# Optimization experiments

Measured on AMD Instinct MI355X. Metric: run time of the kernel, lower is better.

Reference implementation:

```python
import jax, jax.numpy as jnp
import numpy as np

D = 256; HEADS = 8; LVLS = 4; PTS = 4; NLAYERS = 6; DFF = 1024
SHAPES = [(64, 64), (32, 32), (16, 16), (8, 8)]
B = 4
N = sum(h * w for h, w in SHAPES)  # 5440


def setup_inputs() -> dict:
    key = jax.random.key(0)
    ks = jax.random.split(key, 24)
    L = NLAYERS
    w = lambda k, *s: jax.random.normal(k, s, jnp.float32) * 0.02
    inp = {}
    inp['src'] = jax.random.normal(ks[0], (B, N, D), jnp.float32)
    inp['pos'] = jax.random.normal(ks[1], (B, N, D), jnp.float32) * 0.02
    inp['valid_ratios'] = jnp.ones((B, LVLS, 2), jnp.float32)
    inp['spatial_shapes'] = jnp.array(SHAPES, jnp.int32)
    lsi = np.cumsum([0] + [h * w_ for h, w_ in SHAPES])[:-1]
    inp['level_start_index'] = jnp.array(lsi, jnp.int32)
    inp['W_off'] = w(ks[2], L, D, HEADS * LVLS * PTS * 2)
    inp['b_off'] = jax.random.normal(ks[3], (L, HEADS * LVLS * PTS * 2), jnp.float32) * 0.5
    inp['W_attn'] = w(ks[4], L, D, HEADS * LVLS * PTS)
    inp['b_attn'] = jnp.zeros((L, HEADS * LVLS * PTS), jnp.float32)
    inp['W_val'] = w(ks[5], L, D, D)
    inp['b_val'] = jnp.zeros((L, D), jnp.float32)
    inp['W_out'] = w(ks[6], L, D, D)
    inp['b_out'] = jnp.zeros((L, D), jnp.float32)
    inp['g1'] = jnp.ones((L, D), jnp.float32)
    inp['be1'] = jnp.zeros((L, D), jnp.float32)
    inp['W1'] = w(ks[7], L, D, DFF)
    inp['bl1'] = jnp.zeros((L, DFF), jnp.float32)
    inp['W2'] = w(ks[8], L, DFF, D)
    inp['bl2'] = jnp.zeros((L, D), jnp.float32)
    inp['g2'] = jnp.ones((L, D), jnp.float32)
    inp['be2'] = jnp.zeros((L, D), jnp.float32)
    return inp


def layernorm(x, g, b):
    m = x.mean(-1, keepdims=True)
    v = ((x - m) ** 2).mean(-1, keepdims=True)
    return (x - m) * jax.lax.rsqrt(v + 1e-5) * g + b


def get_ref(valid_ratios):
    refs = []
    for lvl, (H_, W_) in enumerate(SHAPES):
        ry, rx = jnp.meshgrid(jnp.linspace(0.5, H_ - 0.5, H_), jnp.linspace(0.5, W_ - 0.5, W_), indexing='ij')
        ry = ry.reshape(-1)[None] / (valid_ratios[:, None, lvl, 1] * H_)
        rx = rx.reshape(-1)[None] / (valid_ratios[:, None, lvl, 0] * W_)
        refs.append(jnp.stack([rx, ry], -1))
    ref = jnp.concatenate(refs, 1)           # [B, N, 2]
    return ref[:, :, None] * valid_ratios[:, None]  # [B, N, L, 2]


def msda(query, value_in, ref, Woff, boff, Wat, bat, Wv, bv, Wo, bo):
    # Standard Deformable-DETR MSDeformAttn (bilinear gather + weighted sum).
    Bq, Q, _ = query.shape
    Dh = D // HEADS
    value = (value_in @ Wv + bv).reshape(Bq, -1, HEADS, Dh).transpose(0, 2, 1, 3)  # [B,H,N,Dh]
    off = (query @ Woff + boff).reshape(Bq, Q, HEADS, LVLS, PTS, 2)
    attn = jax.nn.softmax((query @ Wat + bat).reshape(Bq, Q, HEADS, LVLS * PTS), -1)
    attn = attn.reshape(Bq, Q, HEADS, LVLS, PTS)
    norm = jnp.array([[w_, h_] for h_, w_ in SHAPES], query.dtype)  # (W_, H_) per level
    loc = ref[:, :, None, :, None, :] + off / norm[None, None, None, :, None, :]
    out = jnp.zeros((Bq, Q, HEADS, Dh), query.dtype)
    start = 0
    for lvl, (H_, W_) in enumerate(SHAPES):
        v = value[:, :, start:start + H_ * W_]  # [B,H,HW,Dh]
        start += H_ * W_
        l = loc[:, :, :, lvl]                    # [B,Q,H,P,2] in [0,1]
        x = l[..., 0] * W_ - 0.5
        y = l[..., 1] * H_ - 0.5
        x0 = jnp.floor(x); y0 = jnp.floor(y)
        fx = x - x0; fy = y - y0
        x0i = x0.astype(jnp.int32); y0i = y0.astype(jnp.int32)

        def g(xi, yi):
            valid = ((xi >= 0) & (xi < W_) & (yi >= 0) & (yi < H_)).astype(query.dtype)
            idx = jnp.clip(yi, 0, H_ - 1) * W_ + jnp.clip(xi, 0, W_ - 1)
            it = idx.transpose(0, 2, 1, 3).reshape(Bq, HEADS, -1)  # [B,H,Q*P]
            got = jnp.take_along_axis(v, it[..., None], axis=2)    # [B,H,Q*P,Dh]
            got = got.reshape(Bq, HEADS, Q, PTS, Dh).transpose(0, 2, 1, 3, 4)
            return got * valid[..., None]

        samp = (g(x0i, y0i) * ((1 - fx) * (1 - fy))[..., None]
                + g(x0i + 1, y0i) * (fx * (1 - fy))[..., None]
                + g(x0i, y0i + 1) * ((1 - fx) * fy)[..., None]
                + g(x0i + 1, y0i + 1) * (fx * fy)[..., None])  # [B,Q,H,P,Dh]
        out = out + jnp.einsum('bqhp,bqhpd->bqhd', attn[:, :, :, lvl], samp)
    return out.reshape(Bq, Q, D) @ Wo + bo


def reference(src, pos, valid_ratios, spatial_shapes, level_start_index,
              W_off, b_off, W_attn, b_attn, W_val, b_val, W_out, b_out,
              g1, be1, W1, bl1, W2, bl2, g2, be2):
    ref = get_ref(valid_ratios)
    out = src
    for i in range(NLAYERS):
        q = out + pos
        x2 = msda(q, out, ref, W_off[i], b_off[i], W_attn[i], b_attn[i],
                  W_val[i], b_val[i], W_out[i], b_out[i])
        out = layernorm(out + x2, g1[i], be1[i])
        ffn = jax.nn.relu(out @ W1[i] + bl1[i]) @ W2[i] + bl2[i]
        out = layernorm(out + ffn, g2[i], be2[i])
    return out
```

## Files before the change

### kernel.cpp

```cpp
#include <hip/hip_runtime.h>
#include <math.h>

#define B_   4
#define N_   5440
#define D_   256
#define M_   21760
#define NL_  6
#define MH_  10880

typedef unsigned short us16;
typedef unsigned int   u32;
typedef __attribute__((ext_vector_type(8))) short  short8v;
typedef __attribute__((ext_vector_type(4))) float  f32x4;

__device__ __forceinline__ float b2f(us16 u) {
  return __uint_as_float(((u32)u) << 16);
}
__device__ __forceinline__ int iclip(int v, int lo, int hi) {
  return v < lo ? lo : (v > hi ? hi : v);
}

__global__ __launch_bounds__(256) void split_wT(const float* __restrict__ W,
                                                us16* __restrict__ out,
                                                int K, int N, int ld, int rowOff) {
  const int idx = blockIdx.x * 256 + threadIdx.x;
  const int k = idx % K;
  const int n = (idx / K) % N;
  const int l = idx / (K * N);
  const float x = W[(size_t)l * K * N + (size_t)k * N + n];
  const u32 u = __float_as_uint(x);
  const us16 hi = (us16)(u >> 16);
  const float rem = x - __uint_as_float(u & 0xFFFF0000u);
  const us16 lo = (us16)(__float_as_uint(rem) >> 16);
  us16* o = out + (size_t)l * ld * 2 * K + (size_t)(rowOff + n) * 2 * K;
  o[k] = hi;
  o[K + k] = lo;
}


__global__ __launch_bounds__(256) void gemm_qkv(
    const float* __restrict__ X, const float* __restrict__ P,
    const us16* __restrict__ BT,
    const float* __restrict__ bVal, const float* __restrict__ bOff,
    const float* __restrict__ bAttn,
    float* __restrict__ val, us16* __restrict__ off16,
    us16* __restrict__ attnl16) {
  __shared__ __align__(16) us16 Ah[128 * 72];
  __shared__ __align__(16) us16 Al[128 * 72];
  __shared__ __align__(16) us16 Bh[128 * 72];
  __shared__ __align__(16) us16 Bl[128 * 72];
  const int tid  = threadIdx.x;
  const int row0 = blockIdx.y * 128;
  const int col0 = blockIdx.x * 128;
  const bool useAdd = (col0 >= 256);
  const int l  = tid & 63;
  const int w  = tid >> 6;
  const int wr = (w >> 1) * 64;
  const int wc = (w & 1) * 64;
  const int lg = l >> 4;
  const int lr = l & 15;
  const int K = 256;

  f32x4 acc[4][4];
#pragma unroll
  for (int m = 0; m < 4; ++m)
#pragma unroll
    for (int n = 0; n < 4; ++n)
#pragma unroll
      for (int j = 0; j < 4; ++j) acc[m][n][j] = 0.f;

  for (int t = 0; t < 4; ++t) {
    const int kB = t << 6;
    __syncthreads();
#pragma unroll
    for (int r = 0; r < 4; ++r) {
      const int id = r * 256 + tid;
      const int row = id >> 3;
      const int cg = id & 7;
      const float* src = &X[(size_t)(row0 + row) * K + kB + cg * 8];
      float4 f0 = *(const float4*)src;
      float4 f1 = *(const float4*)(src + 4);
      if (useAdd) {
        const float* s2 = &P[(size_t)(row0 + row) * K + kB + cg * 8];
        float4 g0 = *(const float4*)s2;
        float4 g1 = *(const float4*)(s2 + 4);
        f0.x += g0.x; f0.y += g0.y; f0.z += g0.z; f0.w += g0.w;
        f1.x += g1.x; f1.y += g1.y; f1.z += g1.z; f1.w += g1.w;
      }
      const float xs[8] = {f0.x, f0.y, f0.z, f0.w, f1.x, f1.y, f1.z, f1.w};
      union { us16 u[8]; uint4 v; } ph, pl;
#pragma unroll
      for (int j = 0; j < 8; ++j) {
        const u32 u = __float_as_uint(xs[j]);
        ph.u[j] = (us16)(u >> 16);
        const float rem = xs[j] - __uint_as_float(u & 0xFFFF0000u);
        pl.u[j] = (us16)(__float_as_uint(rem) >> 16);
      }
      *(uint4*)&Ah[row * 72 + cg * 8] = ph.v;
      *(uint4*)&Al[row * 72 + cg * 8] = pl.v;
    }
#pragma unroll
    for (int r = 0; r < 4; ++r) {
      const int id = r * 256 + tid;
      const int row = id >> 3;
      const int cg = id & 7;
      const us16* brow = &BT[(size_t)(col0 + row) * 512];
      *(uint4*)&Bh[row * 72 + cg * 8] = *(const uint4*)&brow[kB + cg * 8];
      *(uint4*)&Bl[row * 72 + cg * 8] = *(const uint4*)&brow[K + kB + cg * 8];
    }
    __syncthreads();
#pragma unroll
    for (int kk = 0; kk < 2; ++kk) {
      const int ko = kk * 32 + lg * 8;
      short8v ah[4], bb[4], cc[4];
#pragma unroll
      for (int mf = 0; mf < 4; ++mf)
        ah[mf] = *(const short8v*)&Ah[(wr + mf * 16 + lr) * 72 + ko];
#pragma unroll
      for (int nf = 0; nf < 4; ++nf)
        bb[nf] = *(const short8v*)&Bh[(wc + nf * 16 + lr) * 72 + ko];
#pragma unroll
      for (int mf = 0; mf < 4; ++mf)
#pragma unroll
        for (int nf = 0; nf < 4; ++nf)
          acc[mf][nf] = __builtin_amdgcn_mfma_f32_16x16x32_bf16(ah[mf], bb[nf], acc[mf][nf], 0, 0, 0);
#pragma unroll
      for (int nf = 0; nf < 4; ++nf)
        cc[nf] = *(const short8v*)&Bl[(wc + nf * 16 + lr) * 72 + ko];
#pragma unroll
      for (int mf = 0; mf < 4; ++mf)
#pragma unroll
        for (int nf = 0; nf < 4; ++nf)
          acc[mf][nf] = __builtin_amdgcn_mfma_f32_16x16x32_bf16(ah[mf], cc[nf], acc[mf][nf], 0, 0, 0);
#pragma unroll
      for (int mf = 0; mf < 4; ++mf)
        ah[mf] = *(const short8v*)&Al[(wr + mf * 16 + lr) * 72 + ko];
#pragma unroll
      for (int mf = 0; mf < 4; ++mf)
#pragma unroll
        for (int nf = 0; nf < 4; ++nf)
          acc[mf][nf] = __builtin_amdgcn_mfma_f32_16x16x32_bf16(ah[mf], bb[nf], acc[mf][nf], 0, 0, 0);
    }
  }
  float* Cf = nullptr; us16* Ch = nullptr;
  const float* bp; int ldc, csub;
  if (col0 < 256)      { Cf = val;     bp = bVal;  ldc = 256; csub = 0;   }
  else if (col0 < 512) { Ch = off16;   bp = bOff;  ldc = 256; csub = 256; }
  else                 { Ch = attnl16; bp = bAttn; ldc = 128; csub = 512; }
#pragma unroll
  for (int mf = 0; mf < 4; ++mf) {
#pragma unroll
    for (int nf = 0; nf < 4; ++nf) {
      const int cc2 = col0 + wc + nf * 16 + lr - csub;
      const float bvv = bp[cc2];
#pragma unroll
      for (int j = 0; j < 4; ++j) {
        const int row = row0 + wr + mf * 16 + lg * 4 + j;
        const float v = acc[mf][nf][j] + bvv;
        if (Ch) Ch[(size_t)row * ldc + cc2] = (us16)(__float_as_uint(v) >> 16);
        else    Cf[(size_t)row * ldc + cc2] = v;
      }
    }
  }
}

__global__ __launch_bounds__(256) void gemm_split(
    const float* __restrict__ A,
    const us16* __restrict__ BT, const float* __restrict__ bias,
    float* __restrict__ C0, float* __restrict__ C1,
    int Kfull, int kLen, int N, int relu) {
  __shared__ __align__(16) us16 Ah[128 * 72];
  __shared__ __align__(16) us16 Al[128 * 72];
  __shared__ __align__(16) us16 Bh[128 * 72];
  __shared__ __align__(16) us16 Bl[128 * 72];
  const int tid  = threadIdx.x;
  const int row0 = blockIdx.y * 128;
  const int col0 = blockIdx.x * 128;
  const int kOff = blockIdx.z * kLen;
  const int l  = tid & 63;
  const int w  = tid >> 6;
  const int wr = (w >> 1) * 64;
  const int wc = (w & 1) * 64;
  const int lg = l >> 4;
  const int lr = l & 15;

  f32x4 acc[4][4];
#pragma unroll
  for (int m = 0; m < 4; ++m)
#pragma unroll
    for (int n = 0; n < 4; ++n)
#pragma unroll
      for (int j = 0; j < 4; ++j) acc[m][n][j] = 0.f;

  const int T = kLen >> 6;
  for (int t = 0; t < T; ++t) {
    const int kB = kOff + (t << 6);
    __syncthreads();
#pragma unroll
    for (int r = 0; r < 4; ++r) {
      const int id = r * 256 + tid;
      const int row = id >> 3;
      const int cg = id & 7;
      const float* src = &A[(size_t)(row0 + row) * Kfull + kB + cg * 8];
      const float4 f0 = *(const float4*)src;
      const float4 f1 = *(const float4*)(src + 4);
      const float xs[8] = {f0.x, f0.y, f0.z, f0.w, f1.x, f1.y, f1.z, f1.w};
      union { us16 u[8]; uint4 v; } ph, pl;
#pragma unroll
      for (int j = 0; j < 8; ++j) {
        const u32 u = __float_as_uint(xs[j]);
        ph.u[j] = (us16)(u >> 16);
        const float rem = xs[j] - __uint_as_float(u & 0xFFFF0000u);
        pl.u[j] = (us16)(__float_as_uint(rem) >> 16);
      }
      *(uint4*)&Ah[row * 72 + cg * 8] = ph.v;
      *(uint4*)&Al[row * 72 + cg * 8] = pl.v;
    }
#pragma unroll
    for (int r = 0; r < 4; ++r) {
      const int id = r * 256 + tid;
      const int row = id >> 3;
      const int cg = id & 7;
      const us16* brow = &BT[(size_t)(col0 + row) * 2 * Kfull];
      *(uint4*)&Bh[row * 72 + cg * 8] = *(const uint4*)&brow[kB + cg * 8];
      *(uint4*)&Bl[row * 72 + cg * 8] = *(const uint4*)&brow[Kfull + kB + cg * 8];
    }
    __syncthreads();
#pragma unroll
    for (int kk = 0; kk < 2; ++kk) {
      const int ko = kk * 32 + lg * 8;
      short8v ah[4], bb[4], cc[4];
#pragma unroll
      for (int mf = 0; mf < 4; ++mf)
        ah[mf] = *(const short8v*)&Ah[(wr + mf * 16 + lr) * 72 + ko];
#pragma unroll
      for (int nf = 0; nf < 4; ++nf)
        bb[nf] = *(const short8v*)&Bh[(wc + nf * 16 + lr) * 72 + ko];
#pragma unroll
      for (int mf = 0; mf < 4; ++mf)
#pragma unroll
        for (int nf = 0; nf < 4; ++nf)
          acc[mf][nf] = __builtin_amdgcn_mfma_f32_16x16x32_bf16(ah[mf], bb[nf], acc[mf][nf], 0, 0, 0);
#pragma unroll
      for (int nf = 0; nf < 4; ++nf)
        cc[nf] = *(const short8v*)&Bl[(wc + nf * 16 + lr) * 72 + ko];
#pragma unroll
      for (int mf = 0; mf < 4; ++mf)
#pragma unroll
        for (int nf = 0; nf < 4; ++nf)
          acc[mf][nf] = __builtin_amdgcn_mfma_f32_16x16x32_bf16(ah[mf], cc[nf], acc[mf][nf], 0, 0, 0);
#pragma unroll
      for (int mf = 0; mf < 4; ++mf)
        ah[mf] = *(const short8v*)&Al[(wr + mf * 16 + lr) * 72 + ko];
#pragma unroll
      for (int mf = 0; mf < 4; ++mf)
#pragma unroll
        for (int nf = 0; nf < 4; ++nf)
          acc[mf][nf] = __builtin_amdgcn_mfma_f32_16x16x32_bf16(ah[mf], bb[nf], acc[mf][nf], 0, 0, 0);
    }
  }
  float* out = blockIdx.z ? C1 : C0;
  const float* bp = blockIdx.z ? nullptr : bias;
#pragma unroll
  for (int mf = 0; mf < 4; ++mf) {
#pragma unroll
    for (int nf = 0; nf < 4; ++nf) {
      const int col = col0 + wc + nf * 16 + lr;
      const float bvv = bp ? bp[col] : 0.f;
#pragma unroll
      for (int j = 0; j < 4; ++j) {
        const int row = row0 + wr + mf * 16 + lg * 4 + j;
        float v = acc[mf][nf][j] + bvv;
        if (relu) v = fmaxf(v, 0.f);
        out[(size_t)row * N + col] = v;
      }
    }
  }
}

__global__ __launch_bounds__(256) void add_into(float* __restrict__ dst,
                                                const float* __restrict__ src,
                                                int n4) {
  const int i = blockIdx.x * 256 + threadIdx.x;
  if (i < n4) {
    float4 d = ((float4*)dst)[i];
    const float4 s = ((const float4*)src)[i];
    d.x += s.x; d.y += s.y; d.z += s.z; d.w += s.w;
    ((float4*)dst)[i] = d;
  }
}

__global__ __launch_bounds__(256) void msda_sample(const us16* __restrict__ off,
                                                   const us16* __restrict__ attnl,
                                                   const float* __restrict__ val,
                                                   const float* __restrict__ vr,
                                                   float* __restrict__ samp) {
  __shared__ __align__(16) float sw[8][16][4];
  __shared__ __align__(16) int   srow[8][16][4];
  const int lsi[4] = {0, 4096, 5120, 5376};
  const int g    = threadIdx.x >> 5;
  const int lane = threadIdx.x & 31;
  const int gid  = blockIdx.x * 8 + g;
  const int h  = gid & 7;
  const int bq = gid >> 3;
  const int q  = bq % N_;
  const int b  = bq / N_;

  const int lq = (q < 4096) ? 0 : ((q < 5120) ? 1 : ((q < 5376) ? 2 : 3));
  const int qq = q - lsi[lq];
  const int Wq = 64 >> lq;
  const int rq = qq >> (6 - lq);
  const int cq = qq & (Wq - 1);

  const float* vb = vr + b * 8;
  const float rxb = (cq + 0.5f) / (vb[lq * 2 + 0] * (float)Wq);
  const float ryb = (rq + 0.5f) / (vb[lq * 2 + 1] * (float)Wq);

  const int p = lane & 15;
  float lgt = b2f(attnl[(size_t)bq * 128 + h * 16 + p]);
  float mx = lgt;
#pragma unroll
  for (int m = 1; m < 16; m <<= 1) mx = fmaxf(mx, __shfl_xor(mx, m, 16));
  const float e = __expf(lgt - mx);
  float s = e;
#pragma unroll
  for (int m = 1; m < 16; m <<= 1) s += __shfl_xor(s, m, 16);
  const float aw = e / s;

  const us16* ob = off + (size_t)bq * 256 + h * 32;
  const float ox = b2f(ob[2 * p]);
  const float oy = b2f(ob[2 * p + 1]);
  const int lvl = p >> 2;
  const int Wl = 64 >> lvl;
  const float refx = rxb * vb[lvl * 2 + 0];
  const float refy = ryb * vb[lvl * 2 + 1];
  const float px = refx * (float)Wl + ox - 0.5f;
  const float py = refy * (float)Wl + oy - 0.5f;
  const float x0f = floorf(px), y0f = floorf(py);
  const float fx = px - x0f, fy = py - y0f;
  const int x0 = (int)x0f, y0 = (int)y0f;
  const int x1 = x0 + 1, y1 = y0 + 1;
  const bool vx0 = (x0 >= 0) & (x0 < Wl);
  const bool vx1 = (x1 >= 0) & (x1 < Wl);
  const bool vy0 = (y0 >= 0) & (y0 < Wl);
  const bool vy1 = (y1 >= 0) & (y1 < Wl);
  float w00 = (1.f - fx) * (1.f - fy) * aw; if (!(vx0 & vy0)) w00 = 0.f;
  float w10 = fx * (1.f - fy) * aw;         if (!(vx1 & vy0)) w10 = 0.f;
  float w01 = (1.f - fx) * fy * aw;         if (!(vx0 & vy1)) w01 = 0.f;
  float w11 = fx * fy * aw;                 if (!(vx1 & vy1)) w11 = 0.f;
  const int xc0 = iclip(x0, 0, Wl - 1), xc1 = iclip(x1, 0, Wl - 1);
  const int yc0 = iclip(y0, 0, Wl - 1), yc1 = iclip(y1, 0, Wl - 1);
  const int rowb = b * N_ + lsi[lvl];
  if (lane < 16) {
    *(float4*)&sw[g][p][0]  = make_float4(w00, w10, w01, w11);
    *(int4*)&srow[g][p][0]  = make_int4(rowb + yc0 * Wl + xc0,
                                        rowb + yc0 * Wl + xc1,
                                        rowb + yc1 * Wl + xc0,
                                        rowb + yc1 * Wl + xc1);
  }
  const float* vcol = val + h * 32 + lane;
  float acc = 0.f;
#pragma unroll
  for (int pp = 0; pp < 16; ++pp) {
    const float4 wv = *(const float4*)&sw[g][pp][0];
    const int4   rv = *(const int4*)&srow[g][pp][0];
    acc += wv.x * vcol[rv.x * 256];
    acc += wv.y * vcol[rv.y * 256];
    acc += wv.z * vcol[rv.z * 256];
    acc += wv.w * vcol[rv.w * 256];
  }
  samp[(size_t)bq * 256 + h * 32 + lane] = acc;
}

__global__ __launch_bounds__(256) void resid_ln(const float* __restrict__ x,
                                                const float* __restrict__ y,
                                                const float* __restrict__ g,
                                                const float* __restrict__ be,
                                                float* __restrict__ out) {
  __shared__ float red[8];
  const int row = blockIdx.x;
  const int t = threadIdx.x;
  const size_t idx = (size_t)row * 256 + t;
  const float v = x[idx] + y[idx];

  float s = v;
#pragma unroll
  for (int o = 1; o < 64; o <<= 1) s += __shfl_xor(s, o, 64);
  const int wid = t >> 6;
  if ((t & 63) == 0) red[wid] = s;
  __syncthreads();
  const float mean = (red[0] + red[1] + red[2] + red[3]) * (1.f / 256.f);
  const float d = v - mean;
  float s2 = d * d;
#pragma unroll
  for (int o = 1; o < 64; o <<= 1) s2 += __shfl_xor(s2, o, 64);
  if ((t & 63) == 0) red[4 + wid] = s2;
  __syncthreads();
  const float var = (red[4] + red[5] + red[6] + red[7]) * (1.f / 256.f);
  out[idx] = d * rsqrtf(var + 1e-5f) * g[t] + be[t];
}

extern "C" void kernel_launch(void* const* d_in, const int* in_sizes, int n_in,
                              void* d_out, int out_size, void* d_ws, size_t ws_size,
                              hipStream_t stream) {
  const float* src    = (const float*)d_in[0];
  const float* pos    = (const float*)d_in[1];
  const float* vr     = (const float*)d_in[2];
  const float* W_off  = (const float*)d_in[5];
  const float* b_off  = (const float*)d_in[6];
  const float* W_attn = (const float*)d_in[7];
  const float* b_attn = (const float*)d_in[8];
  const float* W_val  = (const float*)d_in[9];
  const float* b_val  = (const float*)d_in[10];
  const float* W_out  = (const float*)d_in[11];
  const float* b_out  = (const float*)d_in[12];
  const float* g1     = (const float*)d_in[13];
  const float* be1    = (const float*)d_in[14];
  const float* W1     = (const float*)d_in[15];
  const float* bl1    = (const float*)d_in[16];
  const float* W2     = (const float*)d_in[17];
  const float* bl2    = (const float*)d_in[18];
  const float* g2     = (const float*)d_in[19];
  const float* be2    = (const float*)d_in[20];

  const size_t XD = (size_t)M_ * 256;
  float* ws = (float*)d_ws;
  float* x  = ws;
  float* y  = ws + XD;
  float* R  = ws + 2 * XD;
  us16*  off16   = (us16*)R;
  us16*  attnl16 = (us16*)(R + (size_t)M_ * 128);
  float* val     = R + (size_t)M_ * 192;
  float* samp    = R + (size_t)M_ * 448;
  float* hbuf    = R;
  float* y2      = R + (size_t)M_ * 512;
  us16*  wreg    = (us16*)(R + (size_t)M_ * 704);
  us16* wCat  = wreg;
  us16* wOut  = wCat + 6 * 327680;
  us16* w1s   = wOut + 6 * 131072;
  us16* w2s   = w1s  + 6 * 524288;

  const dim3 blk(256);
  split_wT<<<6 * 256 * 256 / 256, blk, 0, stream>>>(W_val,  wCat, 256, 256, 640, 0);
  split_wT<<<6 * 256 * 256 / 256, blk, 0, stream>>>(W_off,  wCat, 256, 256, 640, 256);
  split_wT<<<6 * 256 * 128 / 256, blk, 0, stream>>>(W_attn, wCat, 256, 128, 640, 512);
  split_wT<<<6 * 256 * 256 / 256, blk, 0, stream>>>(W_out,  wOut, 256, 256, 256, 0);
  split_wT<<<6 * 256 * 1024 / 256, blk, 0, stream>>>(W1,    w1s,  256, 1024, 1024, 0);
  split_wT<<<6 * 1024 * 256 / 256, blk, 0, stream>>>(W2,    w2s,  1024, 256, 256, 0);

  const float* xc = src;
  for (int i = 0; i < NL_; ++i) {
    gemm_qkv<<<dim3(5, 170), blk, 0, stream>>>(
        xc, pos, wCat + (size_t)i * 327680,
        b_val + i * 256, b_off + i * 256, b_attn + i * 128,
        val, off16, attnl16);
    msda_sample<<<M_, blk, 0, stream>>>(off16, attnl16, val, vr, samp);
    gemm_split<<<dim3(2, 170, 1), blk, 0, stream>>>(
        samp, wOut + (size_t)i * 131072, b_out + i * 256, y, nullptr,
        256, 256, 256, 0);
    resid_ln<<<M_, blk, 0, stream>>>(xc, y, g1 + i * 256, be1 + i * 256, x);
    for (int half = 0; half < 2; ++half) {
      const size_t ro = (size_t)half * MH_;
      gemm_split<<<dim3(8, 85, 1), blk, 0, stream>>>(
          x + ro * 256, w1s + (size_t)i * 524288, bl1 + i * 1024,
          hbuf, nullptr, 256, 256, 1024, 1);
      gemm_split<<<dim3(2, 85, 2), blk, 0, stream>>>(
          hbuf, w2s + (size_t)i * 524288, bl2 + i * 256,
          y + ro * 256, y2, 1024, 512, 256, 0);
      add_into<<<(MH_ * 64 + 255) / 256, blk, 0, stream>>>(
          y + ro * 256, y2, MH_ * 64);
    }
    float* dst = (i == NL_ - 1) ? (float*)d_out : x;
    resid_ln<<<M_, blk, 0, stream>>>(x, y, g2 + i * 256, be2 + i * 256, dst);
    xc = x;
  }
}
```

Measured before the change: 2.512 ms.

## Prefetch GEMM tiles into registers and fold split-K partial sums into layernorm

Both GEMM kernels now load the next K-tile's global data into registers while the current tile is being computed, a register-level double buffer that hides global load latency behind the MFMA work. The separate add_into pass over the FFN2 split-K partials is removed: resid_ln3 sums both partial outputs inside the residual layernorm. The output projection also switches to a two-way split-K that reuses the same fused reduction, and the second partial buffer is aliased onto d_out. The cost is higher register pressure from the prefetch buffers, which may reduce occupancy, plus extra partial-sum writes for the output projection.

```diff
diff --git a/kernel.cpp b/kernel.cpp
--- a/kernel.cpp
+++ b/kernel.cpp
@@ -60,6 +60,8 @@
   const int lg = l >> 4;
   const int lr = l & 15;
   const int K = 256;
+  const int arow = tid >> 3;
+  const int acg  = tid & 7;
 
   f32x4 acc[4][4];
 #pragma unroll
@@ -69,21 +71,33 @@
 #pragma unroll
       for (int j = 0; j < 4; ++j) acc[m][n][j] = 0.f;
 
-  for (int t = 0; t < 4; ++t) {
+  float4 rA[8]; float4 rP[8]; uint4 rB[8];
+
+  auto LOAD = [&](int t) {
     const int kB = t << 6;
-    __syncthreads();
 #pragma unroll
     for (int r = 0; r < 4; ++r) {
-      const int id = r * 256 + tid;
-      const int row = id >> 3;
-      const int cg = id & 7;
-      const float* src = &X[(size_t)(row0 + row) * K + kB + cg * 8];
-      float4 f0 = *(const float4*)src;
-      float4 f1 = *(const float4*)(src + 4);
+      const int row = arow + r * 32;
+      const float* src = &X[(size_t)(row0 + row) * K + kB + acg * 8];
+      rA[2 * r]     = *(const float4*)src;
+      rA[2 * r + 1] = *(const float4*)(src + 4);
       if (useAdd) {
-        const float* s2 = &P[(size_t)(row0 + row) * K + kB + cg * 8];
-        float4 g0 = *(const float4*)s2;
-        float4 g1 = *(const float4*)(s2 + 4);
+        const float* s2 = &P[(size_t)(row0 + row) * K + kB + acg * 8];
+        rP[2 * r]     = *(const float4*)s2;
+        rP[2 * r + 1] = *(const float4*)(s2 + 4);
+      }
+      const us16* brow = &BT[(size_t)(col0 + row) * 512];
+      rB[2 * r]     = *(const uint4*)&brow[kB + acg * 8];
+      rB[2 * r + 1] = *(const uint4*)&brow[K + kB + acg * 8];
+    }
+  };
+  auto STORE = [&]() {
+#pragma unroll
+    for (int r = 0; r < 4; ++r) {
+      const int row = arow + r * 32;
+      float4 f0 = rA[2 * r], f1 = rA[2 * r + 1];
+      if (useAdd) {
+        const float4 g0 = rP[2 * r], g1 = rP[2 * r + 1];
         f0.x += g0.x; f0.y += g0.y; f0.z += g0.z; f0.w += g0.w;
         f1.x += g1.x; f1.y += g1.y; f1.z += g1.z; f1.w += g1.w;
       }
@@ -96,18 +110,18 @@
         const float rem = xs[j] - __uint_as_float(u & 0xFFFF0000u);
         pl.u[j] = (us16)(__float_as_uint(rem) >> 16);
       }
-      *(uint4*)&Ah[row * 72 + cg * 8] = ph.v;
-      *(uint4*)&Al[row * 72 + cg * 8] = pl.v;
-    }
-#pragma unroll
-    for (int r = 0; r < 4; ++r) {
-      const int id = r * 256 + tid;
-      const int row = id >> 3;
-      const int cg = id & 7;
-      const us16* brow = &BT[(size_t)(col0 + row) * 512];
-      *(uint4*)&Bh[row * 72 + cg * 8] = *(const uint4*)&brow[kB + cg * 8];
-      *(uint4*)&Bl[row * 72 + cg * 8] = *(const uint4*)&brow[K + kB + cg * 8];
-    }
+      *(uint4*)&Ah[row * 72 + acg * 8] = ph.v;
+      *(uint4*)&Al[row * 72 + acg * 8] = pl.v;
+      *(uint4*)&Bh[row * 72 + acg * 8] = rB[2 * r];
+      *(uint4*)&Bl[row * 72 + acg * 8] = rB[2 * r + 1];
+    }
+  };
+
+  LOAD(0);
+  for (int t = 0; t < 4; ++t) {
+    __syncthreads();
+    STORE();
+    if (t < 3) LOAD(t + 1);
     __syncthreads();
 #pragma unroll
     for (int kk = 0; kk < 2; ++kk) {
@@ -183,6 +197,8 @@
   const int wc = (w & 1) * 64;
   const int lg = l >> 4;
   const int lr = l & 15;
+  const int arow = tid >> 3;
+  const int acg  = tid & 7;
 
   f32x4 acc[4][4];
 #pragma unroll
@@ -192,18 +208,26 @@
 #pragma unroll
       for (int j = 0; j < 4; ++j) acc[m][n][j] = 0.f;
 
-  const int T = kLen >> 6;
-  for (int t = 0; t < T; ++t) {
+  float4 rA[8]; uint4 rB[8];
+
+  auto LOAD = [&](int t) {
     const int kB = kOff + (t << 6);
-    __syncthreads();
 #pragma unroll
     for (int r = 0; r < 4; ++r) {
-      const int id = r * 256 + tid;
-      const int row = id >> 3;
-      const int cg = id & 7;
-      const float* src = &A[(size_t)(row0 + row) * Kfull + kB + cg * 8];
-      const float4 f0 = *(const float4*)src;
-      const float4 f1 = *(const float4*)(src + 4);
+      const int row = arow + r * 32;
+      const float* src = &A[(size_t)(row0 + row) * Kfull + kB + acg * 8];
+      rA[2 * r]     = *(const float4*)src;
+      rA[2 * r + 1] = *(const float4*)(src + 4);
+      const us16* brow = &BT[(size_t)(col0 + row) * 2 * Kfull];
+      rB[2 * r]     = *(const uint4*)&brow[kB + acg * 8];
+      rB[2 * r + 1] = *(const uint4*)&brow[Kfull + kB + acg * 8];
+    }
+  };
+  auto STORE = [&]() {
+#pragma unroll
+    for (int r = 0; r < 4; ++r) {
+      const int row = arow + r * 32;
+      const float4 f0 = rA[2 * r], f1 = rA[2 * r + 1];
       const float xs[8] = {f0.x, f0.y, f0.z, f0.w, f1.x, f1.y, f1.z, f1.w};
       union { us16 u[8]; uint4 v; } ph, pl;
 #pragma unroll
@@ -213,18 +237,19 @@
         const float rem = xs[j] - __uint_as_float(u & 0xFFFF0000u);
         pl.u[j] = (us16)(__float_as_uint(rem) >> 16);
       }
-      *(uint4*)&Ah[row * 72 + cg * 8] = ph.v;
-      *(uint4*)&Al[row * 72 + cg * 8] = pl.v;
-    }
-#pragma unroll
-    for (int r = 0; r < 4; ++r) {
-      const int id = r * 256 + tid;
-      const int row = id >> 3;
-      const int cg = id & 7;
-      const us16* brow = &BT[(size_t)(col0 + row) * 2 * Kfull];
-      *(uint4*)&Bh[row * 72 + cg * 8] = *(const uint4*)&brow[kB + cg * 8];
-      *(uint4*)&Bl[row * 72 + cg * 8] = *(const uint4*)&brow[Kfull + kB + cg * 8];
-    }
+      *(uint4*)&Ah[row * 72 + acg * 8] = ph.v;
+      *(uint4*)&Al[row * 72 + acg * 8] = pl.v;
+      *(uint4*)&Bh[row * 72 + acg * 8] = rB[2 * r];
+      *(uint4*)&Bl[row * 72 + acg * 8] = rB[2 * r + 1];
+    }
+  };
+
+  const int T = kLen >> 6;
+  LOAD(0);
+  for (int t = 0; t < T; ++t) {
+    __syncthreads();
+    STORE();
+    if (t + 1 < T) LOAD(t + 1);
     __syncthreads();
 #pragma unroll
     for (int kk = 0; kk < 2; ++kk) {
@@ -275,18 +300,6 @@
         out[(size_t)row * N + col] = v;
       }
     }
-  }
-}
-
-__global__ __launch_bounds__(256) void add_into(float* __restrict__ dst,
-                                                const float* __restrict__ src,
-                                                int n4) {
-  const int i = blockIdx.x * 256 + threadIdx.x;
-  if (i < n4) {
-    float4 d = ((float4*)dst)[i];
-    const float4 s = ((const float4*)src)[i];
-    d.x += s.x; d.y += s.y; d.z += s.z; d.w += s.w;
-    ((float4*)dst)[i] = d;
   }
 }
 
@@ -372,16 +385,17 @@
   samp[(size_t)bq * 256 + h * 32 + lane] = acc;
 }
 
-__global__ __launch_bounds__(256) void resid_ln(const float* __restrict__ x,
-                                                const float* __restrict__ y,
-                                                const float* __restrict__ g,
-                                                const float* __restrict__ be,
-                                                float* __restrict__ out) {
+__global__ __launch_bounds__(256) void resid_ln3(const float* __restrict__ x,
+                                                 const float* __restrict__ y,
+                                                 const float* __restrict__ y2,
+                                                 const float* __restrict__ g,
+                                                 const float* __restrict__ be,
+                                                 float* __restrict__ out) {
   __shared__ float red[8];
   const int row = blockIdx.x;
   const int t = threadIdx.x;
   const size_t idx = (size_t)row * 256 + t;
-  const float v = x[idx] + y[idx];
+  const float v = x[idx] + y[idx] + y2[idx];
 
   float s = v;
 #pragma unroll
@@ -433,7 +447,7 @@
   float* val     = R + (size_t)M_ * 192;
   float* samp    = R + (size_t)M_ * 448;
   float* hbuf    = R;
-  float* y2      = R + (size_t)M_ * 512;
+  float* y2      = (float*)d_out;
   us16*  wreg    = (us16*)(R + (size_t)M_ * 704);
   us16* wCat  = wreg;
   us16* wOut  = wCat + 6 * 327680;
@@ -455,10 +469,10 @@
         b_val + i * 256, b_off + i * 256, b_attn + i * 128,
         val, off16, attnl16);
     msda_sample<<<M_, blk, 0, stream>>>(off16, attnl16, val, vr, samp);
-    gemm_split<<<dim3(2, 170, 1), blk, 0, stream>>>(
-        samp, wOut + (size_t)i * 131072, b_out + i * 256, y, nullptr,
-        256, 256, 256, 0);
-    resid_ln<<<M_, blk, 0, stream>>>(xc, y, g1 + i * 256, be1 + i * 256, x);
+    gemm_split<<<dim3(2, 170, 2), blk, 0, stream>>>(
+        samp, wOut + (size_t)i * 131072, b_out + i * 256, y, y2,
+        256, 128, 256, 0);
+    resid_ln3<<<M_, blk, 0, stream>>>(xc, y, y2, g1 + i * 256, be1 + i * 256, x);
     for (int half = 0; half < 2; ++half) {
       const size_t ro = (size_t)half * MH_;
       gemm_split<<<dim3(8, 85, 1), blk, 0, stream>>>(
@@ -466,12 +480,10 @@
           hbuf, nullptr, 256, 256, 1024, 1);
       gemm_split<<<dim3(2, 85, 2), blk, 0, stream>>>(
           hbuf, w2s + (size_t)i * 524288, bl2 + i * 256,
-          y + ro * 256, y2, 1024, 512, 256, 0);
-      add_into<<<(MH_ * 64 + 255) / 256, blk, 0, stream>>>(
-          y + ro * 256, y2, MH_ * 64);
+          y + ro * 256, y2 + ro * 256, 1024, 512, 256, 0);
     }
     float* dst = (i == NL_ - 1) ? (float*)d_out : x;
-    resid_ln<<<M_, blk, 0, stream>>>(x, y, g2 + i * 256, be2 + i * 256, dst);
+    resid_ln3<<<M_, blk, 0, stream>>>(x, y, y2, g2 + i * 256, be2 + i * 256, dst);
     xc = x;
   }
 }
```

Result: slower. 2.646 ms (+5.3%).
